# Kernel tuning notes

Hardware: AMD Instinct MI355X
Metric: run time of the kernel (lower is better)

The kernel has to match this reference:

```python
import jax, jax.numpy as jnp
import numpy as np

B, T, C = 4, 1024, 1024
N = 64          # head_size
H = C // N      # 16 heads
DW, DA, DV, DG = 64, 64, 64, 160


def setup_inputs() -> dict:
    key = jax.random.key(0)
    ks = iter(jax.random.split(key, 40))
    rn = lambda shape, s=1.0: jax.random.normal(next(ks), shape, dtype=jnp.float32) * s
    ru = lambda shape: jax.random.uniform(next(ks), shape, dtype=jnp.float32)
    cs = 0.5 / (C ** 0.5)
    return {
        "x": rn((B, T, C)),
        "v_first": rn((B, T, C)),
        "x_r": ru((1, 1, C)), "x_w": ru((1, 1, C)), "x_k": ru((1, 1, C)),
        "x_v": ru((1, 1, C)), "x_a": ru((1, 1, C)), "x_g": ru((1, 1, C)),
        "w0": rn((1, 1, C), 0.3) - 1.0,
        "w1": rn((C, DW), 0.05), "w2": rn((DW, C), 0.05),
        "a0": rn((1, 1, C), 0.3) - 0.19,
        "a1": rn((C, DA), 0.05), "a2": rn((DA, C), 0.05),
        "v0": rn((1, 1, C), 0.3) + 0.73,
        "v1": rn((C, DV), 0.05), "v2": rn((DV, C), 0.05),
        "g1": rn((C, DG), 0.05), "g2": rn((DG, C), 0.05),
        "k_k": ru((1, 1, C)) * 0.2 + 0.6,
        "k_a": ru((1, 1, C)) * 0.2 + 0.9,
        "r_k": rn((H, N), 0.05) - 0.04,
        "Wr": rn((C, C), cs), "Wk": rn((C, C), 0.1 * cs),
        "Wv": rn((C, C), cs), "Wo": rn((C, C), 0.02),
        "gn_w": jnp.ones((C,), jnp.float32), "gn_b": jnp.zeros((C,), jnp.float32),
        "ln_w": jnp.ones((C,), jnp.float32), "ln_b": jnp.zeros((C,), jnp.float32),
    }


def reference(x, v_first, x_r, x_w, x_k, x_v, x_a, x_g,
              w0, w1, w2, a0, a1, a2, v0, v1, v2, g1, g2,
              k_k, k_a, r_k, Wr, Wk, Wv, Wo, gn_w, gn_b, ln_w, ln_b):
    Bb, Tt, Cc = x.shape
    # ZeroPad2d((0,0,1,-1)): shift tokens right by one along T, then subtract x
    xx = jnp.concatenate([jnp.zeros_like(x[:, :1]), x[:, :-1]], axis=1) - x
    xr = x + xx * x_r; xw = x + xx * x_w; xkk = x + xx * x_k
    xv = x + xx * x_v; xa = x + xx * x_a; xg = x + xx * x_g

    r = xr @ Wr.T                                                    # [B,T,C]
    w = -jax.nn.softplus(-(w0 + jnp.tanh(xw @ w1) @ w2)) - 0.5       # log-decay <= -0.5
    k = xkk @ Wk.T
    v = xv @ Wv.T
    # layer_id=1 != 0 -> value residual mixing with v_first
    v = v + (v_first - v) * jax.nn.sigmoid(v0 + (xv @ v1) @ v2)
    a = jax.nn.sigmoid(a0 + (xa @ a1) @ a2)
    g = jax.nn.sigmoid(xg @ g1) @ g2

    kk = (k * k_k).reshape(Bb, Tt, H, N)
    kk = kk / jnp.maximum(jnp.linalg.norm(kk, axis=-1, keepdims=True), 1e-12)
    kk = kk.reshape(Bb, Tt, Cc)
    k = k * (1.0 + (a - 1.0) * k_a)

    # RWKV-7 generalized delta rule scan: kernel args (r, w, k, v, -kk, kk*a)
    decay = jnp.exp(-jnp.exp(w))                                     # [B,T,C]
    aa = -kk
    bb = kk * a
    tbhn = lambda t: t.reshape(Bb, Tt, H, N).transpose(1, 0, 2, 3)   # [T,B,H,N]
    rs, ws, ks_, vs, as_, bs = map(tbhn, (r, decay, k, v, aa, bb))

    S0 = jnp.zeros((Bb, H, N, N), dtype=x.dtype)  # [B,H, value N, key N]

    def step(S, inp):
        r_t, w_t, k_t, v_t, a_t, b_t = inp
        sa = jnp.einsum('bhij,bhj->bhi', S, a_t)                     # removal readout
        S = (S * w_t[:, :, None, :]
             + sa[..., None] * b_t[:, :, None, :]
             + v_t[..., None] * k_t[:, :, None, :])
        y = jnp.einsum('bhij,bhj->bhi', S, r_t)
        return S, (y, sa)

    _, (ys, sas) = jax.lax.scan(step, S0, (rs, ws, ks_, vs, as_, bs))
    x_att = ys.transpose(1, 0, 2, 3).reshape(Bb, Tt, Cc)
    sa_out = sas.transpose(1, 0, 2, 3).reshape(Bb, Tt, Cc)

    # ln_sa: LayerNorm over C (eps 1e-5)
    mu = sa_out.mean(-1, keepdims=True)
    var = sa_out.var(-1, keepdims=True)
    state_rep = (sa_out - mu) / jnp.sqrt(var + 1e-5) * ln_w + ln_b

    # ln_x: GroupNorm(H groups, eps=0.00064) applied per token
    xh = x_att.reshape(Bb, Tt, H, N)
    gm = xh.mean(-1, keepdims=True)
    gv = xh.var(-1, keepdims=True)
    xn = ((xh - gm) / jnp.sqrt(gv + 0.00064)).reshape(Bb, Tt, Cc) * gn_w + gn_b

    rh = r.reshape(Bb, Tt, H, N)
    kh = k.reshape(Bb, Tt, H, N)
    vh = v.reshape(Bb, Tt, H, N)
    bonus = ((rh * kh * r_k).sum(-1, keepdims=True) * vh).reshape(Bb, Tt, Cc)
    x_att = xn + bonus

    out = (x_att * g) @ Wo.T
    return out, v_first, state_rep
```

## Files before the change

kernel.cpp:

```cpp
#include <hip/hip_runtime.h>
#include <hip/hip_bf16.h>
#include <cstdint>
#include <cstddef>

typedef __attribute__((ext_vector_type(8))) short short8;
typedef __attribute__((ext_vector_type(4))) short short4v;
typedef __attribute__((ext_vector_type(4))) float f32x4;

#define DEVINL static __device__ __forceinline__

DEVINL float b2f(unsigned short u) {
    union { unsigned int i; float f; } v; v.i = ((unsigned int)u) << 16; return v.f;
}
DEVINL unsigned short f2b(float f) {
    union { float f; unsigned int i; } v; v.f = f;
    unsigned int x = v.i;
    return (unsigned short)((x + 0x7FFFu + ((x >> 16) & 1u)) >> 16);
}
DEVINL unsigned short f2bh(float f) {
    __hip_bfloat16 h = __float2bfloat16(f);
    union { __hip_bfloat16 h; unsigned short u; } v; v.h = h; return v.u;
}
DEVINL void cv8(short8 h, f32x4& lo, f32x4& hi) {
    #pragma unroll
// ... 427 lines not shown
            float kv = b2f((unsigned short)k4[jj]) * inv;
            h = f2bh(kv);
            okh[jj] = (short)h; okl[jj] = (short)f2bh(kv - b2f(h));
        }
        *(short4v*)&ah[t * 72 + s4] = oah;  *(short4v*)&al[t * 72 + s4] = oal;
        *(short4v*)&bh_[t * 72 + s4] = obh; *(short4v*)&bl_[t * 72 + s4] = obl;
        *(short4v*)&kh[t * 72 + s4] = okh;  *(short4v*)&kl[t * 72 + s4] = okl;
    }
    {
        const int rj = tid & 63, tq = tid >> 6;
        short4v ov;
        #pragma unroll
        for (int u = 0; u < 4; ++u)
            ov[u] = (short)sc[(tq * 4 + u) * 72 + rj];
        *(short4v*)&vt[rj * 72 + tq * 4] = ov;
    }
    __syncthreads();

    const int w = tid >> 6, lane = tid & 63;
    const int r16 = lane & 15, kg = lane >> 4;
    const int rt = w >> 2, ct = w & 3;

    {
        if (ct > rt) {
            #pragma unroll
            for (int r = 0; r < 4; ++r)
                sc[(rt * 16 + kg * 4 + r) * 72 + ct * 16 + r16] = 0;
        } else {
            short8 Ah[2], Al2[2];
            #pragma unroll
            for (int ks = 0; ks < 2; ++ks) {
                Ah[ks]  = *(const short8*)&ah[(rt * 16 + r16) * 72 + ks * 32 + kg * 8];
                Al2[ks] = *(const short8*)&al[(rt * 16 + r16) * 72 + ks * 32 + kg * 8];
            }
            f32x4 aL = (f32x4){0.f, 0.f, 0.f, 0.f};
            f32x4 aK = (f32x4){0.f, 0.f, 0.f, 0.f};
            #pragma unroll
            for (int ks = 0; ks < 2; ++ks) {
                const int so = (ct * 16 + r16) * 72 + ks * 32 + kg * 8;
                short8 Bh = *(const short8*)&bh_[so];
                short8 Bl = *(const short8*)&bl_[so];
                aL = __builtin_amdgcn_mfma_f32_16x16x32_bf16(Ah[ks], Bh, aL, 0, 0, 0);
                aL = __builtin_amdgcn_mfma_f32_16x16x32_bf16(Ah[ks], Bl, aL, 0, 0, 0);
                aL = __builtin_amdgcn_mfma_f32_16x16x32_bf16(Al2[ks], Bh, aL, 0, 0, 0);
                short8 Kh2 = *(const short8*)&kh[so];
                short8 Kl2 = *(const short8*)&kl[so];
                aK = __builtin_amdgcn_mfma_f32_16x16x32_bf16(Ah[ks], Kh2, aK, 0, 0, 0);
                aK = __builtin_amdgcn_mfma_f32_16x16x32_bf16(Ah[ks], Kl2, aK, 0, 0, 0);
                aK = __builtin_amdgcn_mfma_f32_16x16x32_bf16(Al2[ks], Kh2, aK, 0, 0, 0);
            }
            #pragma unroll
            for (int r = 0; r < 4; ++r) {
                const int t = rt * 16 + kg * 4 + r;
                const int s = ct * 16 + r16;
                Lf[t * 72 + s] = (s < t) ? aL[r] : 0.f;
                sc[t * 72 + s] = (s < t) ? f2bh(aK[r]) : (unsigned short)0;
            }
        }
    }
    __syncthreads();

    {
        const int t = tid >> 4, s4 = (tid & 15) * 4;
        #pragma unroll
        for (int jj = 0; jj < 4; ++jj)
            Xf[t * 132 + s4 + jj] = b2f(ah[t * 72 + s4 + jj]) + b2f(al[t * 72 + s4 + jj]);
    }
    {
        f32x4 acc = (f32x4){0.f, 0.f, 0.f, 0.f};
        #pragma unroll
        for (int ks = 0; ks < 2; ++ks) {
            short8 Af = *(const short8*)&sc[(rt * 16 + r16) * 72 + ks * 32 + kg * 8];
            short8 Bf = *(const short8*)&vt[(ct * 16 + r16) * 72 + ks * 32 + kg * 8];
            acc = __builtin_amdgcn_mfma_f32_16x16x32_bf16(Af, Bf, acc, 0, 0, 0);
        }
        #pragma unroll
        for (int r = 0; r < 4; ++r)
            Xf[(rt * 16 + kg * 4 + r) * 132 + 64 + ct * 16 + r16] = acc[r];
    }
    __syncthreads();

    for (int bi = 0; bi < 4; ++bi) {
        if (bi > 0) {
            const int c = tid & 127;
            const int rb = tid >> 7;
            const int t0 = bi * 16 + rb * 2;
            float a0 = Xf[t0 * 132 + c];
            float a1 = Xf[(t0 + 1) * 132 + c];
            for (int s = 0; s < bi * 16; ++s) {
                float xv = Xf[s * 132 + c];
                a0 += Lf[t0 * 72 + s] * xv;
                a1 += Lf[(t0 + 1) * 72 + s] * xv;
            }
            Xf[t0 * 132 + c] = a0;
            Xf[(t0 + 1) * 132 + c] = a1;
            __syncthreads();
        }
        if (w < 2) {
            const int c = w * 64 + lane;
            float xcol[16];
            #pragma unroll
            for (int u = 0; u < 16; ++u) xcol[u] = Xf[(bi * 16 + u) * 132 + c];
            for (int rr = 1; rr < 16; ++rr) {
                float a2 = xcol[rr];
                for (int s = 0; s < rr; ++s)
                    a2 += Lf[(bi * 16 + rr) * 72 + bi * 16 + s] * xcol[s];
                xcol[rr] = a2;
            }
            #pragma unroll
            for (int u = 1; u < 16; ++u) Xf[(bi * 16 + u) * 132 + c] = xcol[u];
        }
        __syncthreads();
    }

    {
        const int rj = tid & 63, tq = tid >> 6;
        float qv[4], sv[4];
        unsigned short bhv[4], blv[4], khv[4], klv[4];
        #pragma unroll
        for (int u = 0; u < 4; ++u) {
            const int t = tq * 4 + u;
            qv[u] = Xf[t * 132 + rj];
            sv[u] = Xf[t * 132 + 64 + rj];
            bhv[u] = bh_[t * 72 + rj];
            blv[u] = bl_[t * 72 + rj];
            khv[u] = kh[t * 72 + rj];
            klv[u] = kl[t * 72 + rj];
        }
        #pragma unroll
        for (int u = 0; u < 4; ++u) {
            const int t = tq * 4 + u;
            Qg[mb + (size_t)t * 64 + rj] = qv[u];
            SAp[base0 + (size_t)t * Cn + rj] = sv[u];
        }
        __syncthreads();
        unsigned short* sath = (unsigned short*)Lf;
        unsigned short* satl = ((unsigned short*)Lf) + 64 * 72;
        short4v oqh, oql, osh, osl, obh, obl, okh, okl;
        #pragma unroll
        for (int u = 0; u < 4; ++u) {
            unsigned short h = f2bh(qv[u]);
            oqh[u] = (short)h; oql[u] = (short)f2bh(qv[u] - b2f(h));
            h = f2bh(sv[u]);
            osh[u] = (short)h; osl[u] = (short)f2bh(sv[u] - b2f(h));
            obh[u] = (short)bhv[u]; obl[u] = (short)blv[u];
            okh[u] = (short)khv[u]; okl[u] = (short)klv[u];
        }
        *(short4v*)&ah[rj * 72 + tq * 4] = oqh;
        *(short4v*)&al[rj * 72 + tq * 4] = oql;
        *(short4v*)&sath[rj * 72 + tq * 4] = osh;
        *(short4v*)&satl[rj * 72 + tq * 4] = osl;
        *(short4v*)&bh_[rj * 72 + tq * 4] = obh;
        *(short4v*)&bl_[rj * 72 + tq * 4] = obl;
        *(short4v*)&kh[rj * 72 + tq * 4] = okh;
        *(short4v*)&kl[rj * 72 + tq * 4] = okl;
    }
    __syncthreads();

    {
        unsigned short* sath = (unsigned short*)Lf;
        unsigned short* satl = ((unsigned short*)Lf) + 64 * 72;
        f32x4 aP = (f32x4){0.f, 0.f, 0.f, 0.f};
        f32x4 aC = (f32x4){0.f, 0.f, 0.f, 0.f};
        #pragma unroll
        for (int ks = 0; ks < 2; ++ks) {
            const int ro = (rt * 16 + r16) * 72 + ks * 32 + kg * 8;
            const int co = (ct * 16 + r16) * 72 + ks * 32 + kg * 8;
            short8 Abh = *(const short8*)&bh_[ro];
            short8 Abl = *(const short8*)&bl_[ro];
            short8 Bqh = *(const short8*)&ah[co];
            short8 Bql = *(const short8*)&al[co];
            aP = __builtin_amdgcn_mfma_f32_16x16x32_bf16(Abh, Bqh, aP, 0, 0, 0);
            aP = __builtin_amdgcn_mfma_f32_16x16x32_bf16(Abh, Bql, aP, 0, 0, 0);
            aP = __builtin_amdgcn_mfma_f32_16x16x32_bf16(Abl, Bqh, aP, 0, 0, 0);
            short8 Ash = *(const short8*)&sath[ro];
            short8 Asl = *(const short8*)&satl[ro];
            short8 Bbh = *(const short8*)&bh_[co];
            short8 Bbl = *(const short8*)&bl_[co];
            aC = __builtin_amdgcn_mfma_f32_16x16x32_bf16(Ash, Bbh, aC, 0, 0, 0);
            aC = __builtin_amdgcn_mfma_f32_16x16x32_bf16(Ash, Bbl, aC, 0, 0, 0);
            aC = __builtin_amdgcn_mfma_f32_16x16x32_bf16(Asl, Bbh, aC, 0, 0, 0);
            short8 Avt = *(const short8*)&vt[ro];
            short8 Bkh = *(const short8*)&kh[co];
            short8 Bkl = *(const short8*)&kl[co];
            aC = __builtin_amdgcn_mfma_f32_16x16x32_bf16(Avt, Bkh, aC, 0, 0, 0);
            aC = __builtin_amdgcn_mfma_f32_16x16x32_bf16(Avt, Bkl, aC, 0, 0, 0);
        }
        #pragma unroll
        for (int r = 0; r < 4; ++r) {
            const int row = rt * 16 + kg * 4 + r;
            const int col = ct * 16 + r16;
            Pg[mb + (size_t)row * 64 + col] = dT[row] * (aP[r] + ((row == col) ? 1.f : 0.f));
            Cg[mb + (size_t)row * 64 + col] = dT[col] * aC[r];
        }
    }
}

__global__ __launch_bounds__(256, 1) void kB_combine(
    const float* __restrict__ Pg, const float* __restrict__ Cg,
    float* __restrict__ Sinit)
{
    __shared__ float Sl[64 * 65];
    __shared__ float PT[64 * 65];
    const int tid = threadIdx.x;
    const int w = tid >> 6;
    const int l = tid & 63;
    const int lr = l & 15;
    const int lg = l >> 4;
    const int bh = blockIdx.x;

    f32x4 acc[4];
    #pragma unroll
    for (int t = 0; t < 4; ++t) acc[t] = (f32x4){0.f, 0.f, 0.f, 0.f};

    f32x4 pr[4]; f32x4 cr[4];
    {
        const size_t ob = (size_t)(bh * 16) * 4096;
        #pragma unroll
        for (int u = 0; u < 4; ++u)
            pr[u] = *(const f32x4*)(Pg + ob + (size_t)tid * 16 + u * 4);
        #pragma unroll
        for (int t = 0; t < 4; ++t)
            #pragma unroll
            for (int r = 0; r < 4; ++r)
                cr[t][r] = Cg[ob + (size_t)(16 * w + 4 * lg + r) * 64 + 16 * t + lr];
    }

    for (int c = 0; c < NCHUNK; ++c) {
        const size_t ob = (size_t)(bh * 16 + c) * 4096;
        #pragma unroll
        for (int t = 0; t < 4; ++t)
            #pragma unroll
            for (int r = 0; r < 4; ++r)
                Sinit[ob + (size_t)(16 * w + 4 * lg + r) * 64 + 16 * t + lr] = acc[t][r];
        if (c == NCHUNK - 1) break;

        #pragma unroll
        for (int t = 0; t < 4; ++t)
            #pragma unroll
            for (int r = 0; r < 4; ++r)
                Sl[(16 * w + 4 * lg + r) * 65 + 16 * t + lr] = acc[t][r];
        {
            const int jr = tid >> 2, j0 = (tid & 3) * 16;
            #pragma unroll
            for (int u = 0; u < 4; ++u)
                #pragma unroll
                for (int e = 0; e < 4; ++e)
                    PT[jr * 65 + j0 + u * 4 + e] = pr[u][e];
        }
        __syncthreads();

        f32x4 prn[4] = {}, crn[4] = {};
        if (c + 1 < NCHUNK - 1) {
            const size_t obn = (size_t)(bh * 16 + c + 1) * 4096;
            #pragma unroll
            for (int u = 0; u < 4; ++u)
                prn[u] = *(const f32x4*)(Pg + obn + (size_t)tid * 16 + u * 4);
            #pragma unroll
            for (int t = 0; t < 4; ++t)
                #pragma unroll
                for (int r = 0; r < 4; ++r)
                    crn[t][r] = Cg[obn + (size_t)(16 * w + 4 * lg + r) * 64 + 16 * t + lr];
        }

        short8 ahi[2], alo[2];
        #pragma unroll
        for (int k0 = 0; k0 < 2; ++k0) {
            const float* sp = &Sl[(16 * w + lr) * 65 + k0 * 32 + lg * 8];
            #pragma unroll
            for (int j = 0; j < 8; ++j) {
                float s = sp[j];
                unsigned short h = f2bh(s);
                ahi[k0][j] = (short)h;
                alo[k0][j] = (short)f2bh(s - b2f(h));
            }
        }

        #pragma unroll
        for (int t = 0; t < 4; ++t) {
            f32x4 nacc = cr[t];
            #pragma unroll
            for (int k0 = 0; k0 < 2; ++k0) {
                short8 bhi, blo;
                const float* pp = &PT[(16 * t + lr) * 65 + k0 * 32 + lg * 8];
                #pragma unroll
                for (int j = 0; j < 8; ++j) {
                    float p = pp[j];
                    unsigned short h = f2bh(p);
                    bhi[j] = (short)h;
                    blo[j] = (short)f2bh(p - b2f(h));
                }
                nacc = __builtin_amdgcn_mfma_f32_16x16x32_bf16(ahi[k0], bhi, nacc, 0, 0, 0);
                nacc = __builtin_amdgcn_mfma_f32_16x16x32_bf16(ahi[k0], blo, nacc, 0, 0, 0);
                nacc = __builtin_amdgcn_mfma_f32_16x16x32_bf16(alo[k0], bhi, nacc, 0, 0, 0);
            }
            acc[t] = nacc;
        }
        __syncthreads();
        #pragma unroll
        for (int u = 0; u < 4; ++u) { pr[u] = prn[u]; cr[u] = crn[u]; }
    }
}

__global__ __launch_bounds__(256) void kD_corr(
    const float* __restrict__ Sinit, const float* __restrict__ Qg,
    float* __restrict__ SAp)
{
    __shared__ float Ql[64 * 65];
    __shared__ float S0l[64 * 65];
    const int tid = threadIdx.x;
    const int bx = blockIdx.x;
    const int bh = bx / 15;
    const int c  = 1 + bx % 15;
    const size_t mb = (size_t)(bh * 16 + c) * 4096;
    const size_t base0 = ((size_t)(bh >> 4) * Tn + (size_t)c * CL) * Cn + (size_t)(bh & 15) * Nn;

    {
        const int r = tid >> 2, c4 = (tid & 3) * 16;
        #pragma unroll
        for (int u = 0; u < 4; ++u) {
            *(f32x4*)&Ql[r * 65 + c4 + u * 4]  = *(const f32x4*)(Qg + mb + (size_t)r * 64 + c4 + u * 4);
            *(f32x4*)&S0l[r * 65 + c4 + u * 4] = *(const f32x4*)(Sinit + mb + (size_t)r * 64 + c4 + u * 4);
        }
    }
    __syncthreads();

    const int w = tid >> 6, l = tid & 63, lr = l & 15, lg = l >> 4;

    short8 qhi[2], qlo[2];
    #pragma unroll
    for (int k0 = 0; k0 < 2; ++k0) {
        const float* qp = &Ql[(16 * w + lr) * 65 + k0 * 32 + lg * 8];
        #pragma unroll
        for (int j = 0; j < 8; ++j) {
            float q = qp[j];
            unsigned short h = f2bh(q);
            qhi[k0][j] = (short)h;
            qlo[k0][j] = (short)f2bh(q - b2f(h));
        }
    }

    #pragma unroll
    for (int tt = 0; tt < 4; ++tt) {
        f32x4 accQ = (f32x4){0.f, 0.f, 0.f, 0.f};
        #pragma unroll
        for (int k0 = 0; k0 < 2; ++k0) {
            short8 bhi, blo;
            const float* sp = &S0l[(16 * tt + lr) * 65 + k0 * 32 + lg * 8];
            #pragma unroll
            for (int j = 0; j < 8; ++j) {
                float s = sp[j];
                unsigned short h = f2bh(s);
                bhi[j] = (short)h;
                blo[j] = (short)f2bh(s - b2f(h));
            }
            accQ = __builtin_amdgcn_mfma_f32_16x16x32_bf16(qhi[k0], bhi, accQ, 0, 0, 0);
            accQ = __builtin_amdgcn_mfma_f32_16x16x32_bf16(qhi[k0], blo, accQ, 0, 0, 0);
            accQ = __builtin_amdgcn_mfma_f32_16x16x32_bf16(qlo[k0], bhi, accQ, 0, 0, 0);
        }
        #pragma unroll
        for (int r = 0; r < 4; ++r) {
            const size_t off = base0 + (size_t)(16 * w + 4 * lg + r) * Cn + 16 * tt + lr;
            SAp[off] += accQ[r];
        }
    }
}

__global__ __launch_bounds__(256) void kY_mfma(
    const float* __restrict__ Wp, const unsigned short* __restrict__ Rp,
    const unsigned short* __restrict__ Kp, const unsigned short* __restrict__ Bbp,
    const unsigned short* __restrict__ Vp,
    const float* __restrict__ SAp, const float* __restrict__ Sinit,
    float* __restrict__ Yp)
{
    __shared__ float Dl[64 * DLD];
    __shared__ unsigned short khS[64 * 72], klS[64 * 72];
    __shared__ unsigned short bhS[64 * 72], blS[64 * 72];
    __shared__ unsigned short vtS[64 * 72];
    __shared__ unsigned short sahS[64 * 72], salS[64 * 72];

    unsigned short* scoreS = (unsigned short*)Dl;
    float* segP = (float*)vtS;

    const int tid = threadIdx.x;
    const int bx = blockIdx.x;
    const int bh = bx >> 4, cc = bx & 15;
    const size_t base0 = ((size_t)(bh >> 4) * Tn + (size_t)cc * CL) * Cn + (size_t)(bh & 15) * Nn;
    const size_t mb = (size_t)bx * 4096;

    float wv[16];
    {
        const int j = tid & 63, seg = tid >> 6;
        float run = 1.f;
        #pragma unroll
        for (int u = 0; u < 16; ++u) {
            wv[u] = Wp[base0 + (size_t)(seg * 16 + u) * Cn + j];
            run *= wv[u];
        }
        segP[seg * 64 + j] = run;
    }
    __syncthreads();
    {
        const int j = tid & 63, seg = tid >> 6;
        float d = 1.f;
        for (int q = 0; q < seg; ++q) d *= segP[q * 64 + j];
        #pragma unroll
        for (int u = 0; u < 16; ++u) {
            d *= wv[u];
            Dl[(seg * 16 + u) * DLD + j] = d;
        }
    }
    __syncthreads();

    const int w = tid >> 6, lane = tid & 63;
    const int r16 = lane & 15, kg = lane >> 4;

    short8 rh[2], rl[2];
    {
        const int t = 16 * w + r16;
        #pragma unroll
        for (int ks = 0; ks < 2; ++ks) {
            const int j0 = ks * 32 + kg * 8;
            short8 rr = *(const short8*)(Rp + base0 + (size_t)t * Cn + j0);
            const float* dp = &Dl[t * DLD + j0];
            #pragma unroll
            for (int jj = 0; jj < 8; ++jj) {
                float rv = b2f((unsigned short)rr[jj]) * dp[jj];
                unsigned short h = f2bh(rv);
                rh[ks][jj] = (short)h;
                rl[ks][jj] = (short)f2bh(rv - b2f(h));
            }
        }
    }

    {
        const int s = tid >> 2, j0 = (tid & 3) * 16;
        const size_t g = base0 + (size_t)s * Cn + j0;
        #pragma unroll
        for (int half = 0; half < 2; ++half) {
            short8 kk8 = *(const short8*)(Kp + g + half * 8);
            short8 bb8 = *(const short8*)(Bbp + g + half * 8);
            short8 okh, okl, obh, obl;
            #pragma unroll
            for (int jj = 0; jj < 8; ++jj) {
                float dd = Dl[s * DLD + j0 + half * 8 + jj];
                float inv = __builtin_amdgcn_rcpf(dd);
                float kv = b2f((unsigned short)kk8[jj]) * inv;
                float bv = b2f((unsigned short)bb8[jj]) * inv;
                unsigned short h1 = f2bh(kv);
                okh[jj] = (short)h1; okl[jj] = (short)f2bh(kv - b2f(h1));
                unsigned short h2 = f2bh(bv);
                obh[jj] = (short)h2; obl[jj] = (short)f2bh(bv - b2f(h2));
            }
            *(short8*)&khS[s * 72 + j0 + half * 8] = okh;
            *(short8*)&klS[s * 72 + j0 + half * 8] = okl;
            *(short8*)&bhS[s * 72 + j0 + half * 8] = obh;
            *(short8*)&blS[s * 72 + j0 + half * 8] = obl;
        }
        const int i0 = (tid & 3) * 16;
        short8 v8a = *(const short8*)(Vp + base0 + (size_t)s * Cn + i0);
        short8 v8b = *(const short8*)(Vp + base0 + (size_t)s * Cn + i0 + 8);
        #pragma unroll
        for (int jj = 0; jj < 8; ++jj) {
            vtS[(i0 + jj) * 72 + s] = (unsigned short)v8a[jj];
            vtS[(i0 + 8 + jj) * 72 + s] = (unsigned short)v8b[jj];
        }
        #pragma unroll
        for (int u = 0; u < 4; ++u) {
            f32x4 sa4 = *(const f32x4*)(SAp + base0 + (size_t)s * Cn + i0 + u * 4);
            #pragma unroll
            for (int e = 0; e < 4; ++e) {
                unsigned short h = f2bh(sa4[e]);
                sahS[(i0 + u * 4 + e) * 72 + s] = h;
                salS[(i0 + u * 4 + e) * 72 + s] = f2bh(sa4[e] - b2f(h));
            }
        }
    }
    __syncthreads();

    f32x4 acc[4];
    #pragma unroll
    for (int ni = 0; ni < 4; ++ni) acc[ni] = (f32x4){0.f, 0.f, 0.f, 0.f};

    #pragma unroll
    for (int ni = 0; ni < 4; ++ni) {
        #pragma unroll
        for (int ks = 0; ks < 2; ++ks) {
            const int i = ni * 16 + r16;
            const int j0 = ks * 32 + kg * 8;
            f32x4 s0a = *(const f32x4*)(Sinit + mb + (size_t)i * 64 + j0);
            f32x4 s0b = *(const f32x4*)(Sinit + mb + (size_t)i * 64 + j0 + 4);
            short8 s0h, s0l;
            #pragma unroll
            for (int jj = 0; jj < 4; ++jj) {
                unsigned short h1 = f2bh(s0a[jj]);
                s0h[jj] = (short)h1; s0l[jj] = (short)f2bh(s0a[jj] - b2f(h1));
                unsigned short h2 = f2bh(s0b[jj]);
                s0h[4 + jj] = (short)h2; s0l[4 + jj] = (short)f2bh(s0b[jj] - b2f(h2));
            }
            acc[ni] = __builtin_amdgcn_mfma_f32_16x16x32_bf16(rh[ks], s0h, acc[ni], 0, 0, 0);
            acc[ni] = __builtin_amdgcn_mfma_f32_16x16x32_bf16(rh[ks], s0l, acc[ni], 0, 0, 0);
            acc[ni] = __builtin_amdgcn_mfma_f32_16x16x32_bf16(rl[ks], s0h, acc[ni], 0, 0, 0);
        }
    }

    #pragma unroll
    for (int si = 0; si < 4; ++si) {
        f32x4 sc2 = (f32x4){0.f, 0.f, 0.f, 0.f};
        #pragma unroll
        for (int ks = 0; ks < 2; ++ks) {
            const int srow = si * 16 + r16;
            const int j0 = ks * 32 + kg * 8;
            short8 kbh = *(const short8*)&khS[srow * 72 + j0];
            short8 kbl = *(const short8*)&klS[srow * 72 + j0];
            sc2 = __builtin_amdgcn_mfma_f32_16x16x32_bf16(rh[ks], kbh, sc2, 0, 0, 0);
            sc2 = __builtin_amdgcn_mfma_f32_16x16x32_bf16(rh[ks], kbl, sc2, 0, 0, 0);
            sc2 = __builtin_amdgcn_mfma_f32_16x16x32_bf16(rl[ks], kbh, sc2, 0, 0, 0);
        }
        const int s = si * 16 + r16;
        #pragma unroll
        for (int r = 0; r < 4; ++r) {
            const int t = 16 * w + kg * 4 + r;
            scoreS[t * 72 + s] = (s <= t) ? f2bh(sc2[r]) : (unsigned short)0;
        }
    }
    #pragma unroll
    for (int ni = 0; ni < 4; ++ni) {
        #pragma unroll
        for (int ks = 0; ks < 2; ++ks) {
            short8 af = *(const short8*)&scoreS[(16 * w + r16) * 72 + ks * 32 + kg * 8];
            short8 vf = *(const short8*)&vtS[(ni * 16 + r16) * 72 + ks * 32 + kg * 8];
            acc[ni] = __builtin_amdgcn_mfma_f32_16x16x32_bf16(af, vf, acc[ni], 0, 0, 0);
        }
    }
    __syncthreads();

    #pragma unroll
    for (int si = 0; si < 4; ++si) {
        f32x4 sc2 = (f32x4){0.f, 0.f, 0.f, 0.f};
        #pragma unroll
        for (int ks = 0; ks < 2; ++ks) {
            const int srow = si * 16 + r16;
            const int j0 = ks * 32 + kg * 8;
            short8 bbh = *(const short8*)&bhS[srow * 72 + j0];
            short8 bbl = *(const short8*)&blS[srow * 72 + j0];
            sc2 = __builtin_amdgcn_mfma_f32_16x16x32_bf16(rh[ks], bbh, sc2, 0, 0, 0);
            sc2 = __builtin_amdgcn_mfma_f32_16x16x32_bf16(rh[ks], bbl, sc2, 0, 0, 0);
            sc2 = __builtin_amdgcn_mfma_f32_16x16x32_bf16(rl[ks], bbh, sc2, 0, 0, 0);
        }
        const int s = si * 16 + r16;
        #pragma unroll
        for (int r = 0; r < 4; ++r) {
            const int t = 16 * w + kg * 4 + r;
            scoreS[t * 72 + s] = (s <= t) ? f2bh(sc2[r]) : (unsigned short)0;
        }
    }
    #pragma unroll
    for (int ni = 0; ni < 4; ++ni) {
        #pragma unroll
        for (int ks = 0; ks < 2; ++ks) {
            short8 af = *(const short8*)&scoreS[(16 * w + r16) * 72 + ks * 32 + kg * 8];
            short8 sh = *(const short8*)&sahS[(ni * 16 + r16) * 72 + ks * 32 + kg * 8];
            short8 sl = *(const short8*)&salS[(ni * 16 + r16) * 72 + ks * 32 + kg * 8];
            acc[ni] = __builtin_amdgcn_mfma_f32_16x16x32_bf16(af, sh, acc[ni], 0, 0, 0);
            acc[ni] = __builtin_amdgcn_mfma_f32_16x16x32_bf16(af, sl, acc[ni], 0, 0, 0);
        }
    }

    #pragma unroll
    for (int ni = 0; ni < 4; ++ni) {
        #pragma unroll
        for (int r = 0; r < 4; ++r) {
            const int t = 16 * w + kg * 4 + r;
            Yp[base0 + (size_t)t * Cn + ni * 16 + r16] = acc[ni][r];
        }
    }
}

__global__ __launch_bounds__(256) void k_elem2(
    const float* __restrict__ Yb, const unsigned short* __restrict__ Rb,
    const unsigned short* __restrict__ Kb, const unsigned short* __restrict__ Vb,
    const unsigned short* __restrict__ Gb,
    const float* __restrict__ gnw, const float* __restrict__ gnb,
    const float* __restrict__ rk,
    unsigned short* __restrict__ AG)
{
    int tid = threadIdx.x;
    size_t gh = (size_t)blockIdx.x * 4 + (tid >> 6);
    int lane = tid & 63;
    int h = (int)(gh & (Hn - 1));
    size_t idx = (gh >> 4) * Cn + (size_t)h * Nn + lane;
    int c = h * Nn + lane;

    float y = Yb[idx];
    float s1 = y, s2 = y * y;
    float p = b2f(Rb[idx]) * b2f(Kb[idx]) * rk[c];
    #pragma unroll
    for (int m = 1; m < 64; m <<= 1) {
        s1 += __shfl_xor(s1, m, 64);
        s2 += __shfl_xor(s2, m, 64);
        p  += __shfl_xor(p, m, 64);
    }
    float mean = s1 * (1.f / 64.f);
    float var = s2 * (1.f / 64.f) - mean * mean;
    float xn = (y - mean) * rsqrtf(var + 0.00064f) * gnw[c] + gnb[c];
    float xatt = xn + p * b2f(Vb[idx]);
    AG[idx] = f2b(xatt * b2f(Gb[idx]));
}

__global__ __launch_bounds__(256) void k_ln(
    const float* __restrict__ SAp,
    const float* __restrict__ lnw, const float* __restrict__ lnb,
    const float* __restrict__ vf_in, float* __restrict__ vf_out,
    float* __restrict__ outp)
{
    __shared__ float red1[4], red2[4];
    int tid = threadIdx.x;
    size_t row = blockIdx.x;
    *(f32x4*)(vf_out + row * Cn + tid * 4) = *(const f32x4*)(vf_in + row * Cn + tid * 4);

    f32x4 v = *(const f32x4*)(SAp + row * Cn + tid * 4);
    float s1 = v[0] + v[1] + v[2] + v[3];
    float s2 = v[0] * v[0] + v[1] * v[1] + v[2] * v[2] + v[3] * v[3];
    #pragma unroll
    for (int m = 1; m < 64; m <<= 1) {
        s1 += __shfl_xor(s1, m, 64);
        s2 += __shfl_xor(s2, m, 64);
    }
    if ((tid & 63) == 0) { red1[tid >> 6] = s1; red2[tid >> 6] = s2; }
    __syncthreads();
    s1 = red1[0] + red1[1] + red1[2] + red1[3];
    s2 = red2[0] + red2[1] + red2[2] + red2[3];
    float mean = s1 * (1.f / 1024.f);
    float var = s2 * (1.f / 1024.f) - mean * mean;
    float rs = rsqrtf(var + 1e-5f);
    f32x4 o;
    #pragma unroll
    for (int u = 0; u < 4; ++u) {
        int c = tid * 4 + u;
        o[u] = (v[u] - mean) * rs * lnw[c] + lnb[c];
    }
    *(f32x4*)(outp + row * Cn + tid * 4) = o;
}

extern "C" void kernel_launch(void* const* d_in, const int* in_sizes, int n_in,
                              void* d_out, int out_size, void* d_ws, size_t ws_size,
                              hipStream_t stream)
{
    (void)in_sizes; (void)n_in; (void)out_size; (void)ws_size;
    const float* x      = (const float*)d_in[0];
    const float* vfirst = (const float*)d_in[1];
    const float* x_r    = (const float*)d_in[2];
    const float* x_w    = (const float*)d_in[3];
    const float* x_k    = (const float*)d_in[4];
    const float* x_v    = (const float*)d_in[5];
    const float* x_a    = (const float*)d_in[6];
    const float* x_g    = (const float*)d_in[7];
    const float* w0     = (const float*)d_in[8];
    const float* w1     = (const float*)d_in[9];
    const float* w2     = (const float*)d_in[10];
    const float* a0     = (const float*)d_in[11];
    const float* a1     = (const float*)d_in[12];
    const float* a2     = (const float*)d_in[13];
    const float* v0     = (const float*)d_in[14];
    const float* v1     = (const float*)d_in[15];
    const float* v2     = (const float*)d_in[16];
    const float* g1     = (const float*)d_in[17];
    const float* g2     = (const float*)d_in[18];
    const float* k_k    = (const float*)d_in[19];
    const float* k_a    = (const float*)d_in[20];
    const float* r_k    = (const float*)d_in[21];
    const float* Wr     = (const float*)d_in[22];
    const float* Wk     = (const float*)d_in[23];
    const float* Wv     = (const float*)d_in[24];
    const float* Wo     = (const float*)d_in[25];
    const float* gn_w   = (const float*)d_in[26];
    const float* gn_b   = (const float*)d_in[27];
    const float* ln_w   = (const float*)d_in[28];
    const float* ln_b   = (const float*)d_in[29];

    char* ws = (char*)d_ws;
    size_t off = 0;
    auto alloc = [&](size_t bytes) -> void* {
        void* p = ws + off;
        off += (bytes + 255) & ~(size_t)255;
        return p;
    };
    unsigned short* Rb  = (unsigned short*)alloc(MX * 2);
    unsigned short* Kb  = (unsigned short*)alloc(MX * 2);
    unsigned short* Vb  = (unsigned short*)alloc(MX * 2);
    unsigned short* SVb = (unsigned short*)alloc(MX * 2);
    unsigned short* Ab  = (unsigned short*)alloc(MX * 2);
    unsigned short* Gb  = (unsigned short*)alloc(MX * 2);
    float* Wdec = (float*)alloc(MX * 4);
    float* Cg   = (float*)alloc(MX * 4);
    float* Pg   = (float*)alloc(MX * 4);
    float* Qg   = (float*)alloc(MX * 4);
    unsigned short* hw = (unsigned short*)alloc((size_t)Mrows * 64 * 2);
    unsigned short* ha = (unsigned short*)alloc((size_t)Mrows * 64 * 2);
    unsigned short* hv = (unsigned short*)alloc((size_t)Mrows * 64 * 2);
    unsigned short* hg = (unsigned short*)alloc((size_t)Mrows * 160 * 2);
    unsigned short* WrB = (unsigned short*)alloc(1048576 * 2);
    unsigned short* WkB = (unsigned short*)alloc(1048576 * 2);
    unsigned short* WvB = (unsigned short*)alloc(1048576 * 2);
    unsigned short* WoB = (unsigned short*)alloc(1048576 * 2);
    unsigned short* w1T = (unsigned short*)alloc(65536 * 2);
    unsigned short* w2T = (unsigned short*)alloc(65536 * 2);
    unsigned short* a1T = (unsigned short*)alloc(65536 * 2);
    unsigned short* a2T = (unsigned short*)alloc(65536 * 2);
    unsigned short* v1T = (unsigned short*)alloc(65536 * 2);
    unsigned short* v2T = (unsigned short*)alloc(65536 * 2);
    unsigned short* g1T = (unsigned short*)alloc(163840 * 2);
    unsigned short* g2T = (unsigned short*)alloc(163840 * 2);

    unsigned short* xrB = (unsigned short*)Cg;
    unsigned short* xkB = (unsigned short*)Cg + MX;
    unsigned short* xvB = (unsigned short*)Wdec;
    unsigned short* xgB = (unsigned short*)Wdec + MX;
    unsigned short* xwB = Ab;
    unsigned short* xaB = Gb;

    float* out_o  = (float*)d_out;
    float* out_vf = out_o + MX;
    float* out_sr = out_o + 2 * MX;
    float* Sinit = out_vf;
    float* Yb    = out_o;
    float* SAb   = out_sr;
    unsigned short* AG = Rb;

    k_prep_all<<<dim3(8960), 256, 0, stream>>>(
        x, x_r, x_w, x_k, x_v, x_a, x_g,
        xrB, xwB, xkB, xvB, xaB, xgB,
        Wr, Wk, Wv, Wo, WrB, WkB, WvB, WoB,
        w1, w2, a1, a2, v1, v2, g1, g2,
        w1T, w2T, a1T, a2T, v1T, v2T, g1T, g2T);

    gemm_small1<<<dim3(16, 3, 4), 256, 0, stream>>>(xwB, xaB, xvB, xgB,
                                                    w1T, a1T, v1T, g1T,
                                                    hw, ha, hv, hg);
    gemm_rkv<<<dim3(32, 8, 3), 256, 0, stream>>>(xrB, xkB, xvB, WrB, WkB, WvB,
                                                 Rb, Kb, Vb);

    gemm_s2<<<dim3(32, 8, 4), 256, 0, stream>>>(hw, ha, hv, hg,
                                                w2T, a2T, v2T, g2T,
                                                Wdec, Ab, SVb, Gb,
                                                w0, a0, v0);

    kA_wy<<<dim3(1024), 1024, 0, stream>>>(Wdec, Kb, Vb, SVb, Ab,
                                           vfirst, k_k, k_a,
                                           Pg, Cg, Qg, SAb);
    kB_combine<<<dim3(64), 256, 0, stream>>>(Pg, Cg, Sinit);
    kD_corr<<<dim3(960), 256, 0, stream>>>(Sinit, Qg, SAb);
    kY_mfma<<<dim3(1024), 256, 0, stream>>>(Wdec, Rb, Kb, Ab, Vb, SAb, Sinit, Yb);

    k_elem2<<<dim3(16384), 256, 0, stream>>>(Yb, Rb, Kb, Vb, Gb, gn_w, gn_b, r_k, AG);

    k_ln<<<dim3(4096), 256, 0, stream>>>(SAb, ln_w, ln_b, vfirst, out_vf, out_sr);
    gemm2<0, 1><<<dim3(32, 8), 256, 0, stream>>>(AG, Cn, WoB, Cn, out_o, nullptr, Cn, nullptr, Cn);
}
```

Baseline: 327.8 us.

## Fuse chunk-state correction kernel into kY_mfma and drop SA low-bf16 split

```diff
diff --git a/kernel.cpp b/kernel.cpp
--- a/kernel.cpp
+++ b/kernel.cpp
@@ -753,84 +753,22 @@
     }
 }
 
-__global__ __launch_bounds__(256) void kD_corr(
-    const float* __restrict__ Sinit, const float* __restrict__ Qg,
-    float* __restrict__ SAp)
-{
-    __shared__ float Ql[64 * 65];
-    __shared__ float S0l[64 * 65];
-    const int tid = threadIdx.x;
-    const int bx = blockIdx.x;
-    const int bh = bx / 15;
-    const int c  = 1 + bx % 15;
-    const size_t mb = (size_t)(bh * 16 + c) * 4096;
-    const size_t base0 = ((size_t)(bh >> 4) * Tn + (size_t)c * CL) * Cn + (size_t)(bh & 15) * Nn;
-
-    {
-        const int r = tid >> 2, c4 = (tid & 3) * 16;
-        #pragma unroll
-        for (int u = 0; u < 4; ++u) {
-            *(f32x4*)&Ql[r * 65 + c4 + u * 4]  = *(const f32x4*)(Qg + mb + (size_t)r * 64 + c4 + u * 4);
-            *(f32x4*)&S0l[r * 65 + c4 + u * 4] = *(const f32x4*)(Sinit + mb + (size_t)r * 64 + c4 + u * 4);
-        }
-    }
-    __syncthreads();
-
-    const int w = tid >> 6, l = tid & 63, lr = l & 15, lg = l >> 4;
-
-    short8 qhi[2], qlo[2];
-    #pragma unroll
-    for (int k0 = 0; k0 < 2; ++k0) {
-        const float* qp = &Ql[(16 * w + lr) * 65 + k0 * 32 + lg * 8];
-        #pragma unroll
-        for (int j = 0; j < 8; ++j) {
-            float q = qp[j];
-            unsigned short h = f2bh(q);
-            qhi[k0][j] = (short)h;
-            qlo[k0][j] = (short)f2bh(q - b2f(h));
-        }
-    }
-
-    #pragma unroll
-    for (int tt = 0; tt < 4; ++tt) {
-        f32x4 accQ = (f32x4){0.f, 0.f, 0.f, 0.f};
-        #pragma unroll
-        for (int k0 = 0; k0 < 2; ++k0) {
-            short8 bhi, blo;
-            const float* sp = &S0l[(16 * tt + lr) * 65 + k0 * 32 + lg * 8];
-            #pragma unroll
-            for (int j = 0; j < 8; ++j) {
-                float s = sp[j];
-                unsigned short h = f2bh(s);
-                bhi[j] = (short)h;
-                blo[j] = (short)f2bh(s - b2f(h));
-            }
-            accQ = __builtin_amdgcn_mfma_f32_16x16x32_bf16(qhi[k0], bhi, accQ, 0, 0, 0);
-            accQ = __builtin_amdgcn_mfma_f32_16x16x32_bf16(qhi[k0], blo, accQ, 0, 0, 0);
-            accQ = __builtin_amdgcn_mfma_f32_16x16x32_bf16(qlo[k0], bhi, accQ, 0, 0, 0);
-        }
-        #pragma unroll
-        for (int r = 0; r < 4; ++r) {
-            const size_t off = base0 + (size_t)(16 * w + 4 * lg + r) * Cn + 16 * tt + lr;
-            SAp[off] += accQ[r];
-        }
-    }
-}
-
 __global__ __launch_bounds__(256) void kY_mfma(
     const float* __restrict__ Wp, const unsigned short* __restrict__ Rp,
     const unsigned short* __restrict__ Kp, const unsigned short* __restrict__ Bbp,
     const unsigned short* __restrict__ Vp,
-    const float* __restrict__ SAp, const float* __restrict__ Sinit,
+    const float* __restrict__ Qg, const float* __restrict__ Sinit,
+    float* __restrict__ SAp,
     float* __restrict__ Yp)
 {
     __shared__ float Dl[64 * DLD];
     __shared__ unsigned short khS[64 * 72], klS[64 * 72];
     __shared__ unsigned short bhS[64 * 72], blS[64 * 72];
     __shared__ unsigned short vtS[64 * 72];
-    __shared__ unsigned short sahS[64 * 72], salS[64 * 72];
+    __shared__ unsigned short sahS[64 * 72];
 
     unsigned short* scoreS = (unsigned short*)Dl;
+    float* SAf = Dl;
     float* segP = (float*)vtS;
 
     const int tid = threadIdx.x;
@@ -907,32 +845,49 @@
             *(short8*)&klS[s * 72 + j0 + half * 8] = okl;
             *(short8*)&bhS[s * 72 + j0 + half * 8] = obh;
             *(short8*)&blS[s * 72 + j0 + half * 8] = obl;
-        }
-        const int i0 = (tid & 3) * 16;
-        short8 v8a = *(const short8*)(Vp + base0 + (size_t)s * Cn + i0);
-        short8 v8b = *(const short8*)(Vp + base0 + (size_t)s * Cn + i0 + 8);
-        #pragma unroll
-        for (int jj = 0; jj < 8; ++jj) {
-            vtS[(i0 + jj) * 72 + s] = (unsigned short)v8a[jj];
-            vtS[(i0 + 8 + jj) * 72 + s] = (unsigned short)v8b[jj];
-        }
-        #pragma unroll
-        for (int u = 0; u < 4; ++u) {
-            f32x4 sa4 = *(const f32x4*)(SAp + base0 + (size_t)s * Cn + i0 + u * 4);
-            #pragma unroll
-            for (int e = 0; e < 4; ++e) {
-                unsigned short h = f2bh(sa4[e]);
-                sahS[(i0 + u * 4 + e) * 72 + s] = h;
-                salS[(i0 + u * 4 + e) * 72 + s] = f2bh(sa4[e] - b2f(h));
-            }
-        }
-    }
-    __syncthreads();
-
-    f32x4 acc[4];
-    #pragma unroll
-    for (int ni = 0; ni < 4; ++ni) acc[ni] = (f32x4){0.f, 0.f, 0.f, 0.f};
-
+            *(short8*)&sahS[s * 72 + j0 + half * 8] =
+                *(const short8*)(Vp + g + half * 8);
+        }
+    }
+    __syncthreads();
+
+    {
+        const int rj = tid & 63, tq = tid >> 6;
+        unsigned short tmp[16];
+        #pragma unroll
+        for (int u = 0; u < 16; ++u)
+            tmp[u] = sahS[(tq * 16 + u) * 72 + rj];
+        short8 o0, o1;
+        #pragma unroll
+        for (int u = 0; u < 8; ++u) { o0[u] = (short)tmp[u]; o1[u] = (short)tmp[8 + u]; }
+        *(short8*)&vtS[rj * 72 + tq * 16] = o0;
+        *(short8*)&vtS[rj * 72 + tq * 16 + 8] = o1;
+    }
+    __syncthreads();
+
+    f32x4 acc[4], accC[4];
+    #pragma unroll
+    for (int ni = 0; ni < 4; ++ni) {
+        acc[ni] = (f32x4){0.f, 0.f, 0.f, 0.f};
+        accC[ni] = (f32x4){0.f, 0.f, 0.f, 0.f};
+    }
+    short8 qh[2], ql[2];
+    if (cc > 0) {
+        const int t = 16 * w + r16;
+        #pragma unroll
+        for (int ks = 0; ks < 2; ++ks) {
+            const int j0 = ks * 32 + kg * 8;
+            f32x4 qa = *(const f32x4*)(Qg + mb + (size_t)t * 64 + j0);
+            f32x4 qb = *(const f32x4*)(Qg + mb + (size_t)t * 64 + j0 + 4);
+            #pragma unroll
+            for (int jj = 0; jj < 4; ++jj) {
+                unsigned short h1 = f2bh(qa[jj]);
+                qh[ks][jj] = (short)h1; ql[ks][jj] = (short)f2bh(qa[jj] - b2f(h1));
+                unsigned short h2 = f2bh(qb[jj]);
+                qh[ks][4 + jj] = (short)h2; ql[ks][4 + jj] = (short)f2bh(qb[jj] - b2f(h2));
+            }
+        }
+    }
     #pragma unroll
     for (int ni = 0; ni < 4; ++ni) {
         #pragma unroll
@@ -952,8 +907,41 @@
             acc[ni] = __builtin_amdgcn_mfma_f32_16x16x32_bf16(rh[ks], s0h, acc[ni], 0, 0, 0);
             acc[ni] = __builtin_amdgcn_mfma_f32_16x16x32_bf16(rh[ks], s0l, acc[ni], 0, 0, 0);
             acc[ni] = __builtin_amdgcn_mfma_f32_16x16x32_bf16(rl[ks], s0h, acc[ni], 0, 0, 0);
-        }
-    }
+            if (cc > 0) {
+                accC[ni] = __builtin_amdgcn_mfma_f32_16x16x32_bf16(qh[ks], s0h, accC[ni], 0, 0, 0);
+                accC[ni] = __builtin_amdgcn_mfma_f32_16x16x32_bf16(qh[ks], s0l, accC[ni], 0, 0, 0);
+                accC[ni] = __builtin_amdgcn_mfma_f32_16x16x32_bf16(ql[ks], s0h, accC[ni], 0, 0, 0);
+            }
+        }
+    }
+
+    #pragma unroll
+    for (int ni = 0; ni < 4; ++ni) {
+        #pragma unroll
+        for (int r = 0; r < 4; ++r) {
+            const int t = 16 * w + kg * 4 + r;
+            const int i = ni * 16 + r16;
+            const size_t off = base0 + (size_t)t * Cn + i;
+            float sa = SAp[off] + accC[ni][r];
+            SAp[off] = sa;
+            SAf[t * 65 + i] = sa;
+        }
+    }
+    __syncthreads();
+
+    {
+        const int rj = tid & 63, tq = tid >> 6;
+        unsigned short tmp[16];
+        #pragma unroll
+        for (int u = 0; u < 16; ++u)
+            tmp[u] = f2bh(SAf[(tq * 16 + u) * 65 + rj]);
+        short8 o0, o1;
+        #pragma unroll
+        for (int u = 0; u < 8; ++u) { o0[u] = (short)tmp[u]; o1[u] = (short)tmp[8 + u]; }
+        *(short8*)&sahS[rj * 72 + tq * 16] = o0;
+        *(short8*)&sahS[rj * 72 + tq * 16 + 8] = o1;
+    }
+    __syncthreads();
 
     #pragma unroll
     for (int si = 0; si < 4; ++si) {
@@ -1012,9 +1000,7 @@
         for (int ks = 0; ks < 2; ++ks) {
             short8 af = *(const short8*)&scoreS[(16 * w + r16) * 72 + ks * 32 + kg * 8];
             short8 sh = *(const short8*)&sahS[(ni * 16 + r16) * 72 + ks * 32 + kg * 8];
-            short8 sl = *(const short8*)&salS[(ni * 16 + r16) * 72 + ks * 32 + kg * 8];
             acc[ni] = __builtin_amdgcn_mfma_f32_16x16x32_bf16(af, sh, acc[ni], 0, 0, 0);
-            acc[ni] = __builtin_amdgcn_mfma_f32_16x16x32_bf16(af, sl, acc[ni], 0, 0, 0);
         }
     }
 
@@ -1201,8 +1187,8 @@
                                            vfirst, k_k, k_a,
                                            Pg, Cg, Qg, SAb);
     kB_combine<<<dim3(64), 256, 0, stream>>>(Pg, Cg, Sinit);
-    kD_corr<<<dim3(960), 256, 0, stream>>>(Sinit, Qg, SAb);
-    kY_mfma<<<dim3(1024), 256, 0, stream>>>(Wdec, Rb, Kb, Ab, Vb, SAb, Sinit, Yb);
+    kY_mfma<<<dim3(1024), 256, 0, stream>>>(Wdec, Rb, Kb, Ab, Vb,
+                                            Qg, Sinit, SAb, Yb);
 
     k_elem2<<<dim3(16384), 256, 0, stream>>>(Yb, Rb, Kb, Vb, Gb, gn_w, gn_b, r_k, AG);
 
```

New measurement: 320.5 us. -2.2%, faster.
